# Optimization experiments

Hardware: AMD Instinct MI355X
Metric: run time of the kernel (lower is better)

Reference implementation:

```python
import jax, jax.numpy as jnp
import numpy as np
from jax import lax

B, L = 2, 1024
D_MODEL, D_STATE, EXPAND, D_CONV = 1024, 16, 2, 4
D_INNER = EXPAND * D_MODEL            # 2048
DT_RANK = (D_MODEL + 15) // 16        # 64


def setup_inputs() -> dict:
    key = jax.random.key(0)
    ks = jax.random.split(key, 8)
    g = lambda k, shape, s=0.02: jax.random.normal(k, shape, dtype=jnp.float32) * s
    # Mamba-style A init: A = -exp(A_log), A_log = log(1..d_state) per channel
    A_log = jnp.log(jnp.broadcast_to(
        jnp.arange(1, D_STATE + 1, dtype=jnp.float32), (D_INNER, D_STATE)))
    return {
        "x": jax.random.normal(ks[0], (B, L, D_MODEL), dtype=jnp.float32),
        "W_in": g(ks[1], (D_MODEL, 2 * D_INNER)),
        "conv_w": g(ks[2], (D_INNER, D_CONV), 0.1),
        "conv_b": jnp.zeros((D_INNER,), jnp.float32),
        "W_x": g(ks[3], (D_INNER, DT_RANK + 2 * D_STATE)),
        "W_dt": g(ks[4], (DT_RANK, D_INNER)),
        "b_dt": g(ks[5], (D_INNER,), 0.1),
        "A_log": A_log,
        "D_skip": jnp.ones((D_INNER,), jnp.float32),
        "W_out": g(ks[6], (D_INNER, D_MODEL)),
    }


def reference(x, W_in, conv_w, conv_b, W_x, W_dt, b_dt, A_log, D_skip, W_out):
    # in_proj -> (u, z): [B, L, D_INNER] each
    xz = x @ W_in
    u, z = xz[..., :D_INNER], xz[..., D_INNER:]

    # causal depthwise conv1d, kernel D_CONV (small fixed loop over taps)
    up = jnp.pad(u, ((0, 0), (D_CONV - 1, 0), (0, 0)))
    u = sum(up[:, k:k + L, :] * conv_w[:, k] for k in range(D_CONV)) + conv_b
    u = jax.nn.silu(u)

    # input-dependent dt, B, C
    x_dbl = u @ W_x                                    # [B, L, dt_rank + 2N]
    dt = x_dbl[..., :DT_RANK]
    Bm = x_dbl[..., DT_RANK:DT_RANK + D_STATE]         # [B, L, N]
    Cm = x_dbl[..., DT_RANK + D_STATE:]                # [B, L, N]
    delta = jax.nn.softplus(dt @ W_dt + b_dt)          # [B, L, D]

    A = -jnp.exp(A_log)                                # [D, N]
    deltaA = jnp.exp(jnp.einsum('bld,dn->bldn', delta, A))   # [B, L, D, N]
    dBu = (delta * u)[..., None] * Bm[:, :, None, :]          # [B, L, D, N]

    def step(h, inp):
        dA_t, dBu_t, c_t = inp                         # [B,D,N],[B,D,N],[B,N]
        h = dA_t * h + dBu_t
        y_t = jnp.einsum('bdn,bn->bd', h, c_t)
        return h, y_t

    h0 = jnp.zeros((B, D_INNER, D_STATE), x.dtype)
    _, ys = lax.scan(step, h0,
                     (deltaA.transpose(1, 0, 2, 3),
                      dBu.transpose(1, 0, 2, 3),
                      Cm.transpose(1, 0, 2)))
    y = ys.transpose(1, 0, 2) + u * D_skip             # [B, L, D_INNER]
    y = y * jax.nn.silu(z)                             # gated output
    return y @ W_out                                   # [B, L, D_MODEL]
```

## Files before the change

### kernel.cpp

```cpp
#include <hip/hip_runtime.h>


typedef unsigned short u16;
typedef unsigned int   u32;

#define B_SZ 2
#define L_SZ 1024
#define DM   1024
#define DI   2048
#define DS   16
#define DTR  64
#define NXD  96
#define NCHUNK 32
#define CL   32
#define KSPLIT 8
#define KC     256

typedef __bf16 bf16x8 __attribute__((ext_vector_type(8)));
typedef float  f32x4  __attribute__((ext_vector_type(4)));

__device__ __forceinline__ u16 f2bf(float f) {
    u32 x = __float_as_uint(f);
    x += 0x7fffu + ((x >> 16) & 1u);
    return (u16)(x >> 16);
}
__device__ __forceinline__ float bf2f(u16 v) {
    return __uint_as_float(((u32)v) << 16);
}

__device__ __forceinline__ void gld_lds16(const u16* g, u16* l) {
    __builtin_amdgcn_global_load_lds(
        (const __attribute__((address_space(1))) u32*)g,
        (__attribute__((address_space(3))) u32*)l, 16, 0, 0);
}

__device__ __forceinline__ void wg_barrier() {
    __asm__ volatile("" ::: "memory");
    __builtin_amdgcn_s_barrier();
    __asm__ volatile("" ::: "memory");
}
#define WAIT_VM12() __builtin_amdgcn_s_waitcnt(0xF7C)
#define WAIT_VM8()  __builtin_amdgcn_s_waitcnt(0xF78)
#define WAIT_VM6()  __builtin_amdgcn_s_waitcnt(0xF76)
#define WAIT_VM4()  __builtin_amdgcn_s_waitcnt(0xF74)
#define WAIT_VM2()  __builtin_amdgcn_s_waitcnt(0xF72)
#define WAIT_VM0()  __builtin_amdgcn_s_waitcnt(0xF70)

__global__ __launch_bounds__(256) void gemm128p(
    const u16* __restrict__ A, const u16* __restrict__ BT,
    float* __restrict__ Cf, u16* __restrict__ Cb,
    int M, int N, int K, int op)
{
    __shared__ u16 As[4][128 * 32];
    __shared__ u16 Bs[4][128 * 32];

    const int tid  = threadIdx.x;
    const int wave = tid >> 6;
    const int lane = tid & 63;
    const int q    = lane >> 4;
    const int r16  = lane & 15;
    const int wm   = (wave & 1) * 64;
    const int wn   = (wave >> 1) * 64;
    const int flat = blockIdx.y * 32 + blockIdx.x;
    const int xcd  = flat & 7;
    const int idx  = flat >> 3;
    const int m0   = (idx >> 2) * 128;
    const int n0   = (xcd * 4 + (idx & 3)) * 128;

    const u16* gA0 = A  + (size_t)(m0 + (tid >> 2))      * K + (tid & 3) * 8;
    const u16* gA1 = A  + (size_t)(m0 + 64 + (tid >> 2)) * K + (tid & 3) * 8;
    const u16* gB0 = BT + (size_t)(n0 + (tid >> 2))      * K + (tid & 3) * 8;
    const u16* gB1 = BT + (size_t)(n0 + 64 + (tid >> 2)) * K + (tid & 3) * 8;

    const int niter = K >> 5;
    const int pre = niter < 3 ? niter : 3;
    for (int p = 0; p < pre; ++p) {
        const int k0 = p * 32;
        gld_lds16(gA0 + k0, &As[p][tid * 8]);
        gld_lds16(gA1 + k0, &As[p][2048 + tid * 8]);
        gld_lds16(gB0 + k0, &Bs[p][tid * 8]);
        gld_lds16(gB1 + k0, &Bs[p][2048 + tid * 8]);
    }

    f32x4 acc[4][4];
#pragma unroll
    for (int s = 0; s < 4; ++s)
#pragma unroll
        for (int j = 0; j < 4; ++j) acc[s][j] = (f32x4){0.f, 0.f, 0.f, 0.f};

    for (int it = 0; it < niter; ++it) {
        if (it + 3 < niter) {
            const int k0 = (it + 3) * 32;
            const int bi = (it + 3) & 3;
            gld_lds16(gA0 + k0, &As[bi][tid * 8]);
            gld_lds16(gA1 + k0, &As[bi][2048 + tid * 8]);
            gld_lds16(gB0 + k0, &Bs[bi][tid * 8]);
            gld_lds16(gB1 + k0, &Bs[bi][2048 + tid * 8]);
            WAIT_VM12();
        } else if (it + 2 < niter) {
            WAIT_VM8();
        } else if (it + 1 < niter) {
            WAIT_VM4();
        } else {
            WAIT_VM0();
        }
        wg_barrier();

        const int cur = it & 3;
        bf16x8 af[4], bfr[4];
#pragma unroll
        for (int s = 0; s < 4; ++s)
            af[s] = *(const bf16x8*)(&As[cur][(wm + s * 16 + r16) * 32 + q * 8]);
#pragma unroll
        for (int j = 0; j < 4; ++j)
            bfr[j] = *(const bf16x8*)(&Bs[cur][(wn + j * 16 + r16) * 32 + q * 8]);
#pragma unroll
        for (int s = 0; s < 4; ++s)
#pragma unroll
            for (int j = 0; j < 4; ++j)
                acc[s][j] = __builtin_amdgcn_mfma_f32_16x16x32_bf16(
                    af[s], bfr[j], acc[s][j], 0, 0, 0);

        wg_barrier();
    }

#pragma unroll
    for (int s = 0; s < 4; ++s) {
        const int row0 = m0 + wm + s * 16 + q * 4;
#pragma unroll
        for (int j = 0; j < 4; ++j) {
            const int col = n0 + wn + j * 16 + r16;
            if (op == 2) {
#pragma unroll
                for (int i = 0; i < 4; ++i)
                    Cb[(size_t)(row0 + i) * N + col] = f2bf(acc[s][j][i]);
            } else {
#pragma unroll
                for (int i = 0; i < 4; ++i)
                    Cf[(size_t)(row0 + i) * N + col] = acc[s][j][i];
            }
        }
    }
}

__global__ __launch_bounds__(256) void gemm_out64(
    const u16* __restrict__ A, const u16* __restrict__ BT,
    float* __restrict__ C, int M, int N, int K)
{
    __shared__ u16 As[4][64 * 32];
    __shared__ u16 Bs[4][64 * 32];

    const int tid  = threadIdx.x;
    const int wave = tid >> 6;
    const int lane = tid & 63;
    const int q    = lane >> 4;
    const int r16  = lane & 15;
    const int wm   = (wave & 1) * 32;
    const int wn   = (wave >> 1) * 32;
    const int flat = blockIdx.y * 16 + blockIdx.x;
    const int xcd  = flat & 7;
    const int idx  = flat >> 3;
    const int n0   = (xcd * 2 + (idx & 1)) * 64;
    const int m0   = (idx >> 1) * 64;

    const u16* gA0 = A  + (size_t)(m0 + (tid >> 2)) * K + (tid & 3) * 8;
    const u16* gB0 = BT + (size_t)(n0 + (tid >> 2)) * K + (tid & 3) * 8;

    const int niter = K >> 5;
    const int pre = niter < 3 ? niter : 3;
    for (int p = 0; p < pre; ++p) {
        const int k0 = p * 32;
        gld_lds16(gA0 + k0, &As[p][tid * 8]);
        gld_lds16(gB0 + k0, &Bs[p][tid * 8]);
    }

    f32x4 acc[2][2];
#pragma unroll
    for (int s = 0; s < 2; ++s)
#pragma unroll
        for (int j = 0; j < 2; ++j) acc[s][j] = (f32x4){0.f, 0.f, 0.f, 0.f};

    for (int it = 0; it < niter; ++it) {
        if (it + 3 < niter) {
            const int k0 = (it + 3) * 32;
            const int bi = (it + 3) & 3;
            gld_lds16(gA0 + k0, &As[bi][tid * 8]);
            gld_lds16(gB0 + k0, &Bs[bi][tid * 8]);
            WAIT_VM6();
        } else if (it + 2 < niter) {
            WAIT_VM4();
        } else if (it + 1 < niter) {
            WAIT_VM2();
        } else {
            WAIT_VM0();
        }
        wg_barrier();

        const int cur = it & 3;
        bf16x8 af[2], bfr[2];
#pragma unroll
        for (int s = 0; s < 2; ++s)
            af[s] = *(const bf16x8*)(&As[cur][(wm + s * 16 + r16) * 32 + q * 8]);
#pragma unroll
        for (int j = 0; j < 2; ++j)
            bfr[j] = *(const bf16x8*)(&Bs[cur][(wn + j * 16 + r16) * 32 + q * 8]);
#pragma unroll
        for (int s = 0; s < 2; ++s)
#pragma unroll
            for (int j = 0; j < 2; ++j)
                acc[s][j] = __builtin_amdgcn_mfma_f32_16x16x32_bf16(
                    af[s], bfr[j], acc[s][j], 0, 0, 0);

        wg_barrier();
    }

#pragma unroll
    for (int s = 0; s < 2; ++s) {
        const int row0 = m0 + wm + s * 16 + q * 4;
#pragma unroll
        for (int j = 0; j < 2; ++j) {
            const int col = n0 + wn + j * 16 + r16;
#pragma unroll
            for (int i = 0; i < 4; ++i)
                C[(size_t)(row0 + i) * N + col] = acc[s][j][i];
        }
    }
}

__global__ __launch_bounds__(256) void gemm_skinny_conv(
    const u16* __restrict__ xzbf, const float* __restrict__ cw,
    const float* __restrict__ cb, const u16* __restrict__ BT,
    float* xdbl, u16* __restrict__ ucbf)
{
    constexpr int LDT = 40;
    __shared__ u16 As[128 * LDT];
    __shared__ u16 Bs[64 * LDT];

    const int tid  = threadIdx.x;
    const int wave = tid >> 6;
    const int lane = tid & 63;
    const int q    = lane >> 4;
    const int r16  = lane & 15;
    const int m0   = blockIdx.y * 128;
    const int n0   = blockIdx.x * 64;
    const int kcs  = blockIdx.z * KC;
    const int sr   = tid >> 2;
    const int ss   = (tid & 3) * 8;

    f32x4 acc[2][4];
#pragma unroll
    for (int s = 0; s < 2; ++s)
#pragma unroll
        for (int j = 0; j < 4; ++j) acc[s][j] = (f32x4){0.f, 0.f, 0.f, 0.f};

    const int bcol  = n0 + sr;
    const int bcolc = bcol < NXD ? bcol : NXD - 1;

    constexpr int NIT = KC / 32;
    for (int it = 0; it < NIT; ++it) {
        const int c = kcs + it * 32 + ss;
        __syncthreads();

        f32x4 cwv[8];
        float cbv[8];
#pragma unroll
        for (int j = 0; j < 8; ++j) {
            cwv[j] = *(const f32x4*)(cw + (size_t)(c + j) * 4);
            cbv[j] = cb[c + j];
        }

        uint4 ua[2];
#pragma unroll
        for (int rsel = 0; rsel < 2; ++rsel) {
            const int r = m0 + rsel * 64 + sr;
            const int l = r & (L_SZ - 1);
            float s8[8];
#pragma unroll
            for (int j = 0; j < 8; ++j) s8[j] = cbv[j];
#pragma unroll
            for (int k = 0; k < 4; ++k) {
                if (l + k - 3 >= 0) {
                    uint4 xv = *(const uint4*)(xzbf + (size_t)(r + k - 3) * (2 * DI) + c);
                    const u16* xp = (const u16*)&xv;
#pragma unroll
                    for (int j = 0; j < 8; ++j) {
                        const float w = (k == 0) ? cwv[j].x : (k == 1) ? cwv[j].y
                                       : (k == 2) ? cwv[j].z : cwv[j].w;
                        s8[j] = fmaf(bf2f(xp[j]), w, s8[j]);
                    }
                }
            }
            u16* up = (u16*)&ua[rsel];
#pragma unroll
            for (int j = 0; j < 8; ++j) {
                float v = s8[j] / (1.f + __expf(-s8[j]));
                up[j] = f2bf(v);
            }
        }
        *(uint4*)(As + sr * LDT + ss)        = ua[0];
        *(uint4*)(As + (64 + sr) * LDT + ss) = ua[1];
        if (n0 == 0) {
            *(uint4*)(ucbf + (size_t)(m0 + sr) * DI + c)      = ua[0];
            *(uint4*)(ucbf + (size_t)(m0 + 64 + sr) * DI + c) = ua[1];
        }
        *(uint4*)(Bs + sr * LDT + ss) =
            *(const uint4*)(BT + (size_t)bcolc * DI + kcs + it * 32 + ss);
        __syncthreads();

        bf16x8 af[2], bfr[4];
#pragma unroll
        for (int s = 0; s < 2; ++s)
            af[s] = *(const bf16x8*)(As + (wave * 32 + s * 16 + r16) * LDT + q * 8);
#pragma unroll
        for (int j = 0; j < 4; ++j)
            bfr[j] = *(const bf16x8*)(Bs + (j * 16 + r16) * LDT + q * 8);
#pragma unroll
        for (int s = 0; s < 2; ++s)
#pragma unroll
            for (int j = 0; j < 4; ++j)
                acc[s][j] = __builtin_amdgcn_mfma_f32_16x16x32_bf16(
                    af[s], bfr[j], acc[s][j], 0, 0, 0);
    }

#pragma unroll
    for (int s = 0; s < 2; ++s) {
        const int row0 = m0 + wave * 32 + s * 16 + q * 4;
#pragma unroll
        for (int j = 0; j < 4; ++j) {
            const int col = n0 + j * 16 + r16;
            if (col < NXD) {
#pragma unroll
                for (int i = 0; i < 4; ++i)
                    atomicAdd(&xdbl[(size_t)(row0 + i) * NXD + col], acc[s][j][i]);
            }
        }
    }
}

__global__ __launch_bounds__(256) void gemm_delta(
    const float* __restrict__ xdbl, const u16* __restrict__ BT,
    const float* __restrict__ bias, float* __restrict__ dlt)
{
    constexpr int LDT = 40;
    __shared__ u16 As[128 * LDT];
    __shared__ u16 Bs[128 * LDT];

    const int tid  = threadIdx.x;
    const int wave = tid >> 6;
    const int lane = tid & 63;
    const int q    = lane >> 4;
    const int r16  = lane & 15;
    const int wm   = (wave & 1) * 64;
    const int wn   = (wave >> 1) * 64;
    const int m0   = blockIdx.y * 128;
    const int n0   = blockIdx.x * 128;
    const int sr   = tid >> 2;
    const int ss   = (tid & 3) * 8;

    f32x4 acc[4][4];
#pragma unroll
    for (int s = 0; s < 4; ++s)
#pragma unroll
        for (int j = 0; j < 4; ++j) acc[s][j] = (f32x4){0.f, 0.f, 0.f, 0.f};

    for (int k0 = 0; k0 < DTR; k0 += 32) {
        __syncthreads();
        f32x4 f0 = *(const f32x4*)(xdbl + (size_t)(m0 + sr) * NXD + k0 + ss);
        f32x4 f1 = *(const f32x4*)(xdbl + (size_t)(m0 + sr) * NXD + k0 + ss + 4);
        f32x4 f2 = *(const f32x4*)(xdbl + (size_t)(m0 + 64 + sr) * NXD + k0 + ss);
        f32x4 f3 = *(const f32x4*)(xdbl + (size_t)(m0 + 64 + sr) * NXD + k0 + ss + 4);
        uint4 bv0 = *(const uint4*)(BT + (size_t)(n0 + sr)      * DTR + k0 + ss);
        uint4 bv1 = *(const uint4*)(BT + (size_t)(n0 + 64 + sr) * DTR + k0 + ss);
        u16* pa0 = As + sr * LDT + ss;
        u16* pa1 = As + (64 + sr) * LDT + ss;
#pragma unroll
        for (int i = 0; i < 4; ++i) { pa0[i] = f2bf(f0[i]); pa0[4 + i] = f2bf(f1[i]); }
#pragma unroll
        for (int i = 0; i < 4; ++i) { pa1[i] = f2bf(f2[i]); pa1[4 + i] = f2bf(f3[i]); }
        *(uint4*)(Bs + sr * LDT + ss)        = bv0;
        *(uint4*)(Bs + (64 + sr) * LDT + ss) = bv1;
        __syncthreads();

        bf16x8 af[4], bfr[4];
#pragma unroll
        for (int s = 0; s < 4; ++s)
            af[s] = *(const bf16x8*)(As + (wm + s * 16 + r16) * LDT + q * 8);
#pragma unroll
        for (int j = 0; j < 4; ++j)
            bfr[j] = *(const bf16x8*)(Bs + (wn + j * 16 + r16) * LDT + q * 8);
#pragma unroll
        for (int s = 0; s < 4; ++s)
#pragma unroll
            for (int j = 0; j < 4; ++j)
                acc[s][j] = __builtin_amdgcn_mfma_f32_16x16x32_bf16(
                    af[s], bfr[j], acc[s][j], 0, 0, 0);
    }

#pragma unroll
    for (int s = 0; s < 4; ++s) {
        const int row0 = m0 + wm + s * 16 + q * 4;
#pragma unroll
        for (int j = 0; j < 4; ++j) {
            const int col = n0 + wn + j * 16 + r16;
            const float bv = bias[col];
#pragma unroll
            for (int i = 0; i < 4; ++i) {
                float v = acc[s][j][i] + bv;
                v = (v > 20.f) ? v : log1pf(__expf(v));
                dlt[(size_t)(row0 + i) * DI + col] = v;
            }
        }
    }
}

__device__ __forceinline__ void tr_tile(
    const float* __restrict__ in, u16* __restrict__ out,
    int R, int C, int tr, int tc, int tid, float (*t)[33])
{
    const int tx = tid & 31, ty = tid >> 5;
    const int r0 = tr * 32, c0 = tc * 32;
#pragma unroll
    for (int i = 0; i < 4; ++i) {
        int r = r0 + ty + i * 8, c = c0 + tx;
        if (r < R && c < C) t[ty + i * 8][tx] = in[(size_t)r * C + c];
    }
    __syncthreads();
#pragma unroll
    for (int i = 0; i < 4; ++i) {
        int oR = c0 + ty + i * 8, oC = r0 + tx;
        if (oR < C && oC < R) out[(size_t)oR * R + oC] = f2bf(t[tx][ty + i * 8]);
    }
}

__global__ __launch_bounds__(256) void prep_kernel(
    const float* __restrict__ x,     u16* __restrict__ xbf,
    const float* __restrict__ W_in,  u16* __restrict__ winT,
    const float* __restrict__ W_out, u16* __restrict__ woutT,
    const float* __restrict__ W_x,   u16* __restrict__ wxT,
    const float* __restrict__ W_dt,  u16* __restrict__ wdtT,
    float* __restrict__ xdbl)
{
    __shared__ float t[32][33];
    const int id  = blockIdx.x;
    const int tid = threadIdx.x;
    if (id < 4096) {
        tr_tile(W_in, winT, 1024, 4096, id >> 7, id & 127, tid, t);
    } else if (id < 6144) {
        int i2 = id - 4096;
        tr_tile(W_out, woutT, 2048, 1024, i2 >> 5, i2 & 31, tid, t);
    } else if (id < 6336) {
        int i3 = id - 6144;
        tr_tile(W_x, wxT, 2048, 96, i3 / 3, i3 % 3, tid, t);
    } else if (id < 6464) {
        int i4 = id - 6336;
        tr_tile(W_dt, wdtT, 64, 2048, i4 >> 6, i4 & 63, tid, t);
    } else if (id < 14656) {
        int i = (id - 6464) * 256 + tid;
        xbf[i] = f2bf(x[i]);
    } else {
        f32x4 z = (f32x4){0.f, 0.f, 0.f, 0.f};
        ((f32x4*)xdbl)[(size_t)(id - 14656) * 256 + tid] = z;
    }
}

__global__ __launch_bounds__(256) void scan_pass1(
    const float* __restrict__ delta, const u16* __restrict__ ucbf,
    const float* __restrict__ xdbl, const float* __restrict__ A_log,
    float* __restrict__ hbuf, float* __restrict__ pbuf)
{
    const int c = blockIdx.x;
    const int d = blockIdx.y * 256 + threadIdx.x;
    const int b = blockIdx.z;
    float Av[16], h[16], P[16];
#pragma unroll
    for (int n = 0; n < 16; ++n) {
        Av[n] = -__expf(A_log[d * 16 + n]);
        h[n] = 0.f; P[n] = 1.f;
    }
    const int rowbase = b * L_SZ + c * CL;
    for (int i = 0; i < CL; ++i) {
        const int row = rowbase + i;
        float dlt = delta[(size_t)row * DI + d];
        float uu  = bf2f(ucbf[(size_t)row * DI + d]);
        float du  = dlt * uu;
        const float* xr = xdbl + (size_t)row * NXD;
#pragma unroll
        for (int n = 0; n < 16; ++n) {
            float e = __expf(dlt * Av[n]);
            P[n] *= e;
            h[n] = fmaf(e, h[n], du * xr[DTR + n]);
        }
    }
    size_t base = ((size_t)((b * NCHUNK + c) * DI + d)) * 16;
#pragma unroll
    for (int n = 0; n < 16; ++n) { hbuf[base + n] = h[n]; pbuf[base + n] = P[n]; }
}

__global__ __launch_bounds__(256) void scan_pass2(
    float* __restrict__ hbuf, const float* __restrict__ pbuf)
{
    const int j = blockIdx.x * 256 + threadIdx.x;
    const int b = blockIdx.y;
    float h0 = 0.f;
    for (int cc = 0; cc < NCHUNK; ++cc) {
        size_t o = ((size_t)(b * NCHUNK + cc)) * (DI * 16) + j;
        float hl = hbuf[o];
        float Pl = pbuf[o];
        hbuf[o] = h0;
        h0 = fmaf(Pl, h0, hl);
    }
}

__global__ __launch_bounds__(256) void scan_pass3(
    const float* __restrict__ delta, const u16* __restrict__ ucbf,
    const float* __restrict__ xdbl, const float* __restrict__ A_log,
    const float* __restrict__ hbuf, const u16* __restrict__ xzbf,
    const float* __restrict__ Dskip, u16* __restrict__ ybf)
{
    const int c = blockIdx.x;
    const int d = blockIdx.y * 256 + threadIdx.x;
    const int b = blockIdx.z;
    float Av[16], h[16];
    size_t base = ((size_t)((b * NCHUNK + c) * DI + d)) * 16;
#pragma unroll
    for (int n = 0; n < 16; ++n) {
        Av[n] = -__expf(A_log[d * 16 + n]);
        h[n]  = hbuf[base + n];
    }
    const float Dk = Dskip[d];
    const int rowbase = b * L_SZ + c * CL;
    for (int i = 0; i < CL; ++i) {
        const int row = rowbase + i;
        float dlt = delta[(size_t)row * DI + d];
        float uu  = bf2f(ucbf[(size_t)row * DI + d]);
        float du  = dlt * uu;
        const float* xr = xdbl + (size_t)row * NXD;
        float y = 0.f;
#pragma unroll
        for (int n = 0; n < 16; ++n) {
            float e = __expf(dlt * Av[n]);
            h[n] = fmaf(e, h[n], du * xr[DTR + n]);
            y = fmaf(h[n], xr[DTR + DS + n], y);
        }
        float zz = bf2f(xzbf[(size_t)row * (2 * DI) + DI + d]);
        float yv = fmaf(uu, Dk, y) * (zz / (1.f + __expf(-zz)));
        ybf[(size_t)row * DI + d] = f2bf(yv);
    }
}

constexpr size_t OFF_DELTA   = 0;
constexpr size_t OFF_XDBL    = OFF_DELTA + 4194304;
constexpr size_t OFF_HBUF    = OFF_XDBL  + 196608;
constexpr size_t OFF_PBUF    = OFF_HBUF  + 2097152;
constexpr size_t OFF_F32_END = OFF_PBUF  + 2097152;
constexpr size_t SOFF_XBF   = 0;
constexpr size_t SOFF_WINT  = SOFF_XBF   + 2097152;
constexpr size_t SOFF_XZBF  = SOFF_WINT  + 4194304;
constexpr size_t SOFF_UCBF  = SOFF_XZBF  + 8388608;
constexpr size_t SOFF_WXT   = SOFF_UCBF  + 4194304;
constexpr size_t SOFF_WDTT  = SOFF_WXT   + 196608;
constexpr size_t SOFF_WOUTT = SOFF_WDTT  + 131072;
constexpr size_t SOFF_YBF   = SOFF_WOUTT + 2097152;

extern "C" void kernel_launch(void* const* d_in, const int* in_sizes, int n_in,
                              void* d_out, int out_size, void* d_ws, size_t ws_size,
                              hipStream_t stream)
{
    const float* x     = (const float*)d_in[0];
    const float* W_in  = (const float*)d_in[1];
    const float* cw    = (const float*)d_in[2];
    const float* cb    = (const float*)d_in[3];
    const float* W_x   = (const float*)d_in[4];
    const float* W_dt  = (const float*)d_in[5];
    const float* b_dt  = (const float*)d_in[6];
    const float* A_log = (const float*)d_in[7];
    const float* Dsk   = (const float*)d_in[8];
    const float* W_out = (const float*)d_in[9];
    float* out = (float*)d_out;

    float* wsf   = (float*)d_ws;
    float* dlt   = wsf + OFF_DELTA;
    float* xdbl  = wsf + OFF_XDBL;
    float* hbuf  = wsf + OFF_HBUF;
    float* pbuf  = wsf + OFF_PBUF;
    u16* sb    = (u16*)(wsf + OFF_F32_END);
    u16* xbf   = sb + SOFF_XBF;
    u16* winT  = sb + SOFF_WINT;
    u16* xzbf  = sb + SOFF_XZBF;
    u16* ucbf  = sb + SOFF_UCBF;
    u16* wxT   = sb + SOFF_WXT;
    u16* wdtT  = sb + SOFF_WDTT;
    u16* woutT = sb + SOFF_WOUTT;
    u16* ybf   = sb + SOFF_YBF;

    prep_kernel<<<14848, 256, 0, stream>>>(x, xbf, W_in, winT, W_out, woutT,
                                           W_x, wxT, W_dt, wdtT, xdbl);

    gemm128p<<<dim3(32, 16), 256, 0, stream>>>(
        xbf, winT, nullptr, xzbf, 2048, 4096, 1024, 2);

    gemm_skinny_conv<<<dim3(2, 16, KSPLIT), 256, 0, stream>>>(
        xzbf, cw, cb, wxT, xdbl, ucbf);

    gemm_delta<<<dim3(16, 16), 256, 0, stream>>>(xdbl, wdtT, b_dt, dlt);

    scan_pass1<<<dim3(NCHUNK, DI / 256, B_SZ), 256, 0, stream>>>(dlt, ucbf, xdbl, A_log, hbuf, pbuf);
    scan_pass2<<<dim3(DI * 16 / 256, B_SZ), 256, 0, stream>>>(hbuf, pbuf);
    scan_pass3<<<dim3(NCHUNK, DI / 256, B_SZ), 256, 0, stream>>>(dlt, ucbf, xdbl, A_log, hbuf, xzbf, Dsk, ybf);

    gemm_out64<<<dim3(16, 32), 256, 0, stream>>>(ybf, woutT, out, 2048, 1024, 2048);
}
```

Baseline: 267.9 us.

## Fuse delta projection and softplus into both scan passes via shared memory

Removes the separate gemm_delta kernel and its 16 MB fp32 delta buffer. Each scan block (32 rows x 256 channels) now computes its own delta tile with MFMA from xdbl and W_dt^T, applies bias and softplus, and stages the result in 32 KB of shared memory. This saves one launch plus the write and two reads of the delta tensor. In exchange the small delta GEMM and its softplus are computed twice, once in pass1 and once in pass3, and each block's shared-memory use grows.

```diff
diff --git a/kernel.cpp b/kernel.cpp
--- a/kernel.cpp
+++ b/kernel.cpp
@@ -332,82 +332,6 @@
 #pragma unroll
                 for (int i = 0; i < 4; ++i)
                     atomicAdd(&xdbl[(size_t)(row0 + i) * NXD + col], acc[s][j][i]);
-            }
-        }
-    }
-}
-
-__global__ __launch_bounds__(256) void gemm_delta(
-    const float* __restrict__ xdbl, const u16* __restrict__ BT,
-    const float* __restrict__ bias, float* __restrict__ dlt)
-{
-    constexpr int LDT = 40;
-    __shared__ u16 As[128 * LDT];
-    __shared__ u16 Bs[128 * LDT];
-
-    const int tid  = threadIdx.x;
-    const int wave = tid >> 6;
-    const int lane = tid & 63;
-    const int q    = lane >> 4;
-    const int r16  = lane & 15;
-    const int wm   = (wave & 1) * 64;
-    const int wn   = (wave >> 1) * 64;
-    const int m0   = blockIdx.y * 128;
-    const int n0   = blockIdx.x * 128;
-    const int sr   = tid >> 2;
-    const int ss   = (tid & 3) * 8;
-
-    f32x4 acc[4][4];
-#pragma unroll
-    for (int s = 0; s < 4; ++s)
-#pragma unroll
-        for (int j = 0; j < 4; ++j) acc[s][j] = (f32x4){0.f, 0.f, 0.f, 0.f};
-
-    for (int k0 = 0; k0 < DTR; k0 += 32) {
-        __syncthreads();
-        f32x4 f0 = *(const f32x4*)(xdbl + (size_t)(m0 + sr) * NXD + k0 + ss);
-        f32x4 f1 = *(const f32x4*)(xdbl + (size_t)(m0 + sr) * NXD + k0 + ss + 4);
-        f32x4 f2 = *(const f32x4*)(xdbl + (size_t)(m0 + 64 + sr) * NXD + k0 + ss);
-        f32x4 f3 = *(const f32x4*)(xdbl + (size_t)(m0 + 64 + sr) * NXD + k0 + ss + 4);
-        uint4 bv0 = *(const uint4*)(BT + (size_t)(n0 + sr)      * DTR + k0 + ss);
-        uint4 bv1 = *(const uint4*)(BT + (size_t)(n0 + 64 + sr) * DTR + k0 + ss);
-        u16* pa0 = As + sr * LDT + ss;
-        u16* pa1 = As + (64 + sr) * LDT + ss;
-#pragma unroll
-        for (int i = 0; i < 4; ++i) { pa0[i] = f2bf(f0[i]); pa0[4 + i] = f2bf(f1[i]); }
-#pragma unroll
-        for (int i = 0; i < 4; ++i) { pa1[i] = f2bf(f2[i]); pa1[4 + i] = f2bf(f3[i]); }
-        *(uint4*)(Bs + sr * LDT + ss)        = bv0;
-        *(uint4*)(Bs + (64 + sr) * LDT + ss) = bv1;
-        __syncthreads();
-
-        bf16x8 af[4], bfr[4];
-#pragma unroll
-        for (int s = 0; s < 4; ++s)
-            af[s] = *(const bf16x8*)(As + (wm + s * 16 + r16) * LDT + q * 8);
-#pragma unroll
-        for (int j = 0; j < 4; ++j)
-            bfr[j] = *(const bf16x8*)(Bs + (wn + j * 16 + r16) * LDT + q * 8);
-#pragma unroll
-        for (int s = 0; s < 4; ++s)
-#pragma unroll
-            for (int j = 0; j < 4; ++j)
-                acc[s][j] = __builtin_amdgcn_mfma_f32_16x16x32_bf16(
-                    af[s], bfr[j], acc[s][j], 0, 0, 0);
-    }
-
-#pragma unroll
-    for (int s = 0; s < 4; ++s) {
-        const int row0 = m0 + wm + s * 16 + q * 4;
-#pragma unroll
-        for (int j = 0; j < 4; ++j) {
-            const int col = n0 + wn + j * 16 + r16;
-            const float bv = bias[col];
-#pragma unroll
-            for (int i = 0; i < 4; ++i) {
-                float v = acc[s][j][i] + bv;
-                v = (v > 20.f) ? v : log1pf(__expf(v));
-                dlt[(size_t)(row0 + i) * DI + col] = v;
             }
         }
     }
@@ -463,24 +387,87 @@
     }
 }
 
+__device__ __forceinline__ void compute_delta_tile(
+    const float* __restrict__ xdbl, const u16* __restrict__ wdtT,
+    const float* __restrict__ b_dt, int rowbase, int d0, int tid,
+    float (*dl)[256])
+{
+    const int wave = tid >> 6;
+    const int lane = tid & 63;
+    const int q    = lane >> 4;
+    const int r16  = lane & 15;
+
+    f32x4 dacc[2][4];
+#pragma unroll
+    for (int mt = 0; mt < 2; ++mt)
+#pragma unroll
+        for (int nt = 0; nt < 4; ++nt) dacc[mt][nt] = (f32x4){0.f, 0.f, 0.f, 0.f};
+
+#pragma unroll
+    for (int ks = 0; ks < 2; ++ks) {
+        bf16x8 afr[2];
+#pragma unroll
+        for (int mt = 0; mt < 2; ++mt) {
+            const float* ap = xdbl + (size_t)(rowbase + mt * 16 + r16) * NXD + ks * 32 + q * 8;
+            f32x4 a0 = *(const f32x4*)ap;
+            f32x4 a1 = *(const f32x4*)(ap + 4);
+            union { u16 u[8]; bf16x8 v; } cvt;
+#pragma unroll
+            for (int i = 0; i < 4; ++i) { cvt.u[i] = f2bf(a0[i]); cvt.u[4 + i] = f2bf(a1[i]); }
+            afr[mt] = cvt.v;
+        }
+#pragma unroll
+        for (int nt = 0; nt < 4; ++nt) {
+            const u16* bp = wdtT + (size_t)(d0 + (wave * 4 + nt) * 16 + r16) * DTR + ks * 32 + q * 8;
+            bf16x8 bfr = *(const bf16x8*)bp;
+#pragma unroll
+            for (int mt = 0; mt < 2; ++mt)
+                dacc[mt][nt] = __builtin_amdgcn_mfma_f32_16x16x32_bf16(
+                    afr[mt], bfr, dacc[mt][nt], 0, 0, 0);
+        }
+    }
+
+#pragma unroll
+    for (int mt = 0; mt < 2; ++mt)
+#pragma unroll
+        for (int nt = 0; nt < 4; ++nt) {
+            const int colg = (wave * 4 + nt) * 16 + r16;
+            const float bv = b_dt[d0 + colg];
+#pragma unroll
+            for (int i = 0; i < 4; ++i) {
+                float v = dacc[mt][nt][i] + bv;
+                v = (v > 20.f) ? v : log1pf(__expf(v));
+                dl[mt * 16 + q * 4 + i][colg] = v;
+            }
+        }
+}
+
 __global__ __launch_bounds__(256) void scan_pass1(
-    const float* __restrict__ delta, const u16* __restrict__ ucbf,
-    const float* __restrict__ xdbl, const float* __restrict__ A_log,
+    const u16* __restrict__ ucbf, const float* __restrict__ xdbl,
+    const u16* __restrict__ wdtT, const float* __restrict__ b_dt,
+    const float* __restrict__ A_log,
     float* __restrict__ hbuf, float* __restrict__ pbuf)
 {
+    __shared__ float dl[CL][256];
     const int c = blockIdx.x;
-    const int d = blockIdx.y * 256 + threadIdx.x;
+    const int g = blockIdx.y;
     const int b = blockIdx.z;
+    const int tid = threadIdx.x;
+    const int d = g * 256 + tid;
+    const int rowbase = b * L_SZ + c * CL;
+
+    compute_delta_tile(xdbl, wdtT, b_dt, rowbase, g * 256, tid, dl);
+    __syncthreads();
+
     float Av[16], h[16], P[16];
 #pragma unroll
     for (int n = 0; n < 16; ++n) {
         Av[n] = -__expf(A_log[d * 16 + n]);
         h[n] = 0.f; P[n] = 1.f;
     }
-    const int rowbase = b * L_SZ + c * CL;
     for (int i = 0; i < CL; ++i) {
         const int row = rowbase + i;
-        float dlt = delta[(size_t)row * DI + d];
+        float dlt = dl[i][tid];
         float uu  = bf2f(ucbf[(size_t)row * DI + d]);
         float du  = dlt * uu;
         const float* xr = xdbl + (size_t)row * NXD;
@@ -512,14 +499,23 @@
 }
 
 __global__ __launch_bounds__(256) void scan_pass3(
-    const float* __restrict__ delta, const u16* __restrict__ ucbf,
-    const float* __restrict__ xdbl, const float* __restrict__ A_log,
-    const float* __restrict__ hbuf, const u16* __restrict__ xzbf,
-    const float* __restrict__ Dskip, u16* __restrict__ ybf)
-{
+    const u16* __restrict__ ucbf, const float* __restrict__ xdbl,
+    const u16* __restrict__ wdtT, const float* __restrict__ b_dt,
+    const float* __restrict__ A_log, const float* __restrict__ hbuf,
+    const u16* __restrict__ xzbf, const float* __restrict__ Dskip,
+    u16* __restrict__ ybf)
+{
+    __shared__ float dl[CL][256];
     const int c = blockIdx.x;
-    const int d = blockIdx.y * 256 + threadIdx.x;
+    const int g = blockIdx.y;
     const int b = blockIdx.z;
+    const int tid = threadIdx.x;
+    const int d = g * 256 + tid;
+    const int rowbase = b * L_SZ + c * CL;
+
+    compute_delta_tile(xdbl, wdtT, b_dt, rowbase, g * 256, tid, dl);
+    __syncthreads();
+
     float Av[16], h[16];
     size_t base = ((size_t)((b * NCHUNK + c) * DI + d)) * 16;
 #pragma unroll
@@ -528,10 +524,9 @@
         h[n]  = hbuf[base + n];
     }
     const float Dk = Dskip[d];
-    const int rowbase = b * L_SZ + c * CL;
     for (int i = 0; i < CL; ++i) {
         const int row = rowbase + i;
-        float dlt = delta[(size_t)row * DI + d];
+        float dlt = dl[i][tid];
         float uu  = bf2f(ucbf[(size_t)row * DI + d]);
         float du  = dlt * uu;
         const float* xr = xdbl + (size_t)row * NXD;
@@ -548,11 +543,10 @@
     }
 }
 
-constexpr size_t OFF_DELTA   = 0;
-constexpr size_t OFF_XDBL    = OFF_DELTA + 4194304;
-constexpr size_t OFF_HBUF    = OFF_XDBL  + 196608;
-constexpr size_t OFF_PBUF    = OFF_HBUF  + 2097152;
-constexpr size_t OFF_F32_END = OFF_PBUF  + 2097152;
+constexpr size_t OFF_XDBL    = 0;
+constexpr size_t OFF_HBUF    = OFF_XDBL + 196608;
+constexpr size_t OFF_PBUF    = OFF_HBUF + 2097152;
+constexpr size_t OFF_F32_END = OFF_PBUF + 2097152;
 constexpr size_t SOFF_XBF   = 0;
 constexpr size_t SOFF_WINT  = SOFF_XBF   + 2097152;
 constexpr size_t SOFF_XZBF  = SOFF_WINT  + 4194304;
@@ -579,7 +573,6 @@
     float* out = (float*)d_out;
 
     float* wsf   = (float*)d_ws;
-    float* dlt   = wsf + OFF_DELTA;
     float* xdbl  = wsf + OFF_XDBL;
     float* hbuf  = wsf + OFF_HBUF;
     float* pbuf  = wsf + OFF_PBUF;
@@ -602,11 +595,11 @@
     gemm_skinny_conv<<<dim3(2, 16, KSPLIT), 256, 0, stream>>>(
         xzbf, cw, cb, wxT, xdbl, ucbf);
 
-    gemm_delta<<<dim3(16, 16), 256, 0, stream>>>(xdbl, wdtT, b_dt, dlt);
-
-    scan_pass1<<<dim3(NCHUNK, DI / 256, B_SZ), 256, 0, stream>>>(dlt, ucbf, xdbl, A_log, hbuf, pbuf);
+    scan_pass1<<<dim3(NCHUNK, DI / 256, B_SZ), 256, 0, stream>>>(
+        ucbf, xdbl, wdtT, b_dt, A_log, hbuf, pbuf);
     scan_pass2<<<dim3(DI * 16 / 256, B_SZ), 256, 0, stream>>>(hbuf, pbuf);
-    scan_pass3<<<dim3(NCHUNK, DI / 256, B_SZ), 256, 0, stream>>>(dlt, ucbf, xdbl, A_log, hbuf, xzbf, Dsk, ybf);
+    scan_pass3<<<dim3(NCHUNK, DI / 256, B_SZ), 256, 0, stream>>>(
+        ucbf, xdbl, wdtT, b_dt, A_log, hbuf, xzbf, Dsk, ybf);
 
     gemm_out64<<<dim3(16, 32), 256, 0, stream>>>(ybf, woutT, out, 2048, 1024, 2048);
 }
```

Result: no change. 270.3 us (+0.9%).
